# Performance work log

Hardware: AMD Instinct MI355X
Metric: run time of the kernel (lower is better)

## Reference

```python
import jax, jax.numpy as jnp
import numpy as np

N = 20000      # nodes
E = 320000     # edges (before self-loops)
D = 128        # esm_embeds
H = 4          # n_heads (layer 1)
G = 256        # graphs in batch
SLOPE = 0.2    # GATConv default negative_slope


def setup_inputs() -> dict:
    key = jax.random.key(0)
    ks = jax.random.split(key, 16)
    x = jax.random.normal(ks[0], (N, D), jnp.float32)
    src = jax.random.randint(ks[1], (E,), 0, N)
    off = jax.random.randint(ks[2], (E,), 1, N)
    dst = (src + off) % N  # guaranteed no self-loops (PyG removes then re-adds them)
    edge_index = jnp.stack([src, dst]).astype(jnp.int64)
    batch = jnp.sort(jax.random.randint(ks[3], (N,), 0, G)).astype(jnp.int64)
    s = 0.05
    W1 = jax.random.normal(ks[4], (D, H * D), jnp.float32) * s
    a_src1 = jax.random.normal(ks[5], (1, H, D), jnp.float32) * s
    a_dst1 = jax.random.normal(ks[6], (1, H, D), jnp.float32) * s
    b1 = jnp.zeros((H * D,), jnp.float32)
    W2 = jax.random.normal(ks[7], (H * D, D), jnp.float32) * s
    a_src2 = jax.random.normal(ks[8], (1, 1, D), jnp.float32) * s
    a_dst2 = jax.random.normal(ks[9], (1, 1, D), jnp.float32) * s
    b2 = jnp.zeros((D,), jnp.float32)
    fc1_w = jax.random.normal(ks[10], (D, 16), jnp.float32) * s
    fc1_b = jnp.zeros((16,), jnp.float32)
    fc2_w = jax.random.normal(ks[11], (16, 1), jnp.float32) * s
    fc2_b = jnp.zeros((1,), jnp.float32)
    return {"x": x, "edge_index": edge_index, "batch": batch,
            "W1": W1, "a_src1": a_src1, "a_dst1": a_dst1, "b1": b1,
            "W2": W2, "a_src2": a_src2, "a_dst2": a_dst2, "b2": b2,
            "fc1_w": fc1_w, "fc1_b": fc1_b, "fc2_w": fc2_w, "fc2_b": fc2_b}


def _gat_conv(h, src, dst, a_src, a_dst, n):
    """h: [n, heads, C]; returns aggregated [n, heads, C] (PyG GATConv message passing)."""
    al_s = jnp.sum(h * a_src, axis=-1)  # [n, heads]
    al_d = jnp.sum(h * a_dst, axis=-1)  # [n, heads]
    e = jax.nn.leaky_relu(al_s[src] + al_d[dst], SLOPE)  # [Etot, heads]
    m = jax.lax.stop_gradient(jax.ops.segment_max(e, dst, num_segments=n))
    ex = jnp.exp(e - m[dst])
    denom = jax.ops.segment_sum(ex, dst, num_segments=n)
    alpha = ex / denom[dst]                               # per-destination softmax
    msg = h[src] * alpha[..., None]                       # [Etot, heads, C]
    return jax.ops.segment_sum(msg, dst, num_segments=n)


def reference(x, edge_index, batch, W1, a_src1, a_dst1, b1,
              W2, a_src2, a_dst2, b2, fc1_w, fc1_b, fc2_w, fc2_b):
    n = x.shape[0]
    loop = jnp.arange(n, dtype=edge_index.dtype)
    src = jnp.concatenate([edge_index[0], loop])  # GATConv add_self_loops=True
    dst = jnp.concatenate([edge_index[1], loop])
    # layer 1: heads=H, concat -> [n, H*D], then ELU (dropout is identity in eval)
    h1 = (x @ W1).reshape(n, H, D)
    o1 = _gat_conv(h1, src, dst, a_src1, a_dst1, n).reshape(n, H * D) + b1
    x1 = jax.nn.elu(o1)
    # layer 2: heads=1, concat -> [n, D], then ReLU
    h2 = (x1 @ W2).reshape(n, 1, D)
    o2 = _gat_conv(h2, src, dst, a_src2, a_dst2, n).reshape(n, D) + b2
    x2 = jax.nn.relu(o2)
    # global max pool over graphs; x2 >= 0 so clamping handles any empty segment
    pooled = jnp.maximum(jax.ops.segment_max(x2, batch, num_segments=G), 0.0)
    hfc = jax.nn.relu(pooled @ fc1_w + fc1_b)
    return hfc @ fc2_w + fc2_b  # [G, 1]
```

## Files before the change

### kernel.cpp

```cpp
#include <hip/hip_runtime.h>
#include <hip/hip_fp16.h>

#define N_NODES 20000
#define E_EDGES 320000
#define D_DIM   128
#define H1HEADS 4
#define G_GRAPHS 256
#define SLOPE   0.2f

typedef _Float16 h8 __attribute__((ext_vector_type(8)));
typedef float float4v __attribute__((ext_vector_type(4)));

__global__ void cnt_k(const int* __restrict__ dst, int* __restrict__ cnt) {
    int e = blockIdx.x * blockDim.x + threadIdx.x;
    if (e < E_EDGES) atomicAdd(&cnt[dst[e]], 1);
}

__global__ __launch_bounds__(256) void scan_k(const int* __restrict__ cnt,
                                              int* __restrict__ rowptr) {
    __shared__ int s[256];
    const int t = threadIdx.x;
    const int CH = (N_NODES + 255) / 256;
    int base = t * CH;
    int sum = 0;
    for (int i = 0; i < CH; ++i) {
        int idx = base + i;
        if (idx < N_NODES) sum += cnt[idx];
    }
    s[t] = sum;
    __syncthreads();
    for (int off = 1; off < 256; off <<= 1) {
        int v = (t >= off) ? s[t - off] : 0;
        __syncthreads();
        s[t] += v;
        __syncthreads();
    }
    int run = (t > 0) ? s[t - 1] : 0;
    for (int i = 0; i < CH; ++i) {
        int idx = base + i;
        if (idx < N_NODES) { rowptr[idx] = run; run += cnt[idx]; }
    }
    if (t == 255) rowptr[N_NODES] = run;
}

__global__ void scat_k(const int* __restrict__ src, const int* __restrict__ dst,
                       const int* __restrict__ rowptr, int* __restrict__ cur,
                       int* __restrict__ csrsrc) {
    int e = blockIdx.x * blockDim.x + threadIdx.x;
    if (e >= E_EDGES) return;
    int d = dst[e];
    int p = rowptr[d] + atomicAdd(&cur[d], 1);
    csrsrc[p] = src[e];
}

__device__ __forceinline__ int bitonic64(int key, int lane) {
#pragma unroll
    for (int k = 2; k <= 64; k <<= 1) {
#pragma unroll
        for (int j = k >> 1; j > 0; j >>= 1) {
            int other = __shfl_xor(key, j);
            bool up = ((lane & k) == 0);
            bool lower = ((lane & j) == 0);
            int mn = min(key, other), mx = max(key, other);
            key = (up == lower) ? mn : mx;
        }
    }
    return key;
}

__global__ __launch_bounds__(256) void sortb_k(const int* __restrict__ rowptr,
                                               int* __restrict__ csrsrc) {
    const int node = (blockIdx.x * blockDim.x + threadIdx.x) >> 6;
    if (node >= N_NODES) return;
    const int lane = threadIdx.x & 63;
    const int r0 = rowptr[node];
    const int deg = rowptr[node + 1] - r0;
    if (deg <= 1 || deg > 64) return;
    int key = 0x7FFFFFFF;
    if (lane < deg) key = csrsrc[r0 + lane];
    key = bitonic64(key, lane);
    if (lane < deg) csrsrc[r0 + lane] = key;
}

__global__ void splitall_k(const float* __restrict__ x, __half* __restrict__ xhi,
                           __half* __restrict__ xlo,
                           const float* __restrict__ W1, __half* __restrict__ w1t,
                           const float* __restrict__ W2, __half* __restrict__ w2t) {
    int i = blockIdx.x * blockDim.x + threadIdx.x;
    if (i < N_NODES * 128) {
        float v = x[i];
        __half h = __float2half(v);
        xhi[i] = h;
        xlo[i] = __float2half(v - __half2float(h));
    }
    if (i < 128 * 512) {
        {
            int k = i >> 9, n = i & 511;
            w1t[n * 128 + k] = __float2half(W1[i]);
        }
        {
            int k = i >> 7, n = i & 127;
            w2t[n * 512 + k] = __float2half(W2[i]);
        }
    }
}

__device__ __forceinline__ void store_val(__half* p, float v) { *p = __float2half(v); }
__device__ __forceinline__ void store_val(float* p, float v) { *p = v; }

template <typename OT>
__global__ __launch_bounds__(256) void fgemm_k(const __half* __restrict__ Ahi,
                                               const __half* __restrict__ Alo,
                                               const __half* __restrict__ BT,
                                               const int M, const int N, const int K,
                                               OT* __restrict__ C) {
    constexpr int SA = 72;
    __shared__ __half Ah[64 * SA], Al[64 * SA];
    const int t = threadIdx.x;
    const int wave = t >> 6, lane = t & 63;
    const int q = lane >> 4, rr = lane & 15;
    const int row0 = blockIdx.x * 64;
    const int col0 = blockIdx.y * 128;
    const int wm = wave & 1, wn = wave >> 1;

    float4v acc[2][4];
#pragma unroll
    for (int i = 0; i < 2; ++i)
#pragma unroll
        for (int j = 0; j < 4; ++j) acc[i][j] = (float4v){0.f, 0.f, 0.f, 0.f};

    for (int kc = 0; kc < K; kc += 64) {
        __syncthreads();
#pragma unroll
        for (int i = 0; i < 2; ++i) {
            int u = t + i * 256;
            int m = u >> 3, mac = u & 7;
            int r = row0 + m;
            uint4 vh = make_uint4(0, 0, 0, 0), vl = make_uint4(0, 0, 0, 0);
            if (r < M) {
                vh = *(const uint4*)(Ahi + (size_t)r * K + kc + mac * 8);
                vl = *(const uint4*)(Alo + (size_t)r * K + kc + mac * 8);
            }
            *(uint4*)(Ah + m * SA + mac * 8) = vh;
            *(uint4*)(Al + m * SA + mac * 8) = vl;
        }
        __syncthreads();
#pragma unroll
        for (int ks = 0; ks < 2; ++ks) {
            const int ko = ks * 32 + q * 8;
            h8 ah[2], alo[2], bh[4];
#pragma unroll
            for (int mt = 0; mt < 2; ++mt) {
                int m = (wm * 2 + mt) * 16 + rr;
                ah[mt]  = *(const h8*)(Ah + m * SA + ko);
                alo[mt] = *(const h8*)(Al + m * SA + ko);
            }
#pragma unroll
            for (int nt = 0; nt < 4; ++nt) {
                int n = (wn * 4 + nt) * 16 + rr;
                bh[nt] = *(const h8*)(BT + (size_t)(col0 + n) * K + kc + ko);
            }
#pragma unroll
            for (int mt = 0; mt < 2; ++mt)
#pragma unroll
                for (int nt = 0; nt < 4; ++nt) {
                    acc[mt][nt] = __builtin_amdgcn_mfma_f32_16x16x32_f16(
                        ah[mt], bh[nt], acc[mt][nt], 0, 0, 0);
                    acc[mt][nt] = __builtin_amdgcn_mfma_f32_16x16x32_f16(
                        alo[mt], bh[nt], acc[mt][nt], 0, 0, 0);
                }
        }
    }
#pragma unroll
    for (int mt = 0; mt < 2; ++mt) {
#pragma unroll
        for (int reg = 0; reg < 4; ++reg) {
            int r = row0 + (wm * 2 + mt) * 16 + q * 4 + reg;
            if (r < M) {
#pragma unroll
                for (int nt = 0; nt < 4; ++nt) {
                    int c = col0 + (wn * 4 + nt) * 16 + rr;
                    store_val(&C[(size_t)r * N + c], acc[mt][nt][reg]);
                }
            }
        }
    }
}

__global__ __launch_bounds__(256) void al16_k(const __half* __restrict__ h,
                                              const float* __restrict__ a_src,
                                              const float* __restrict__ a_dst,
                                              float* __restrict__ als,
                                              float* __restrict__ ald,
                                              const int NH, const int H) {
    int wid = (blockIdx.x * blockDim.x + threadIdx.x) >> 6;
    int lane = threadIdx.x & 63;
    if (wid >= NH) return;
    int hh = wid % H;
    const __half2* row = (const __half2*)(h + (size_t)wid * 128);
    float2 v = __half22float2(row[lane]);
    float2 as2 = ((const float2*)(a_src + hh * 128))[lane];
    float2 ad2 = ((const float2*)(a_dst + hh * 128))[lane];
    float s = v.x * as2.x + v.y * as2.y;
    float d = v.x * ad2.x + v.y * ad2.y;
#pragma unroll
    for (int off = 32; off > 0; off >>= 1) {
        s += __shfl_down(s, off);
        d += __shfl_down(d, off);
    }
    if (lane == 0) { als[wid] = s; ald[wid] = d; }
}

__device__ __forceinline__ float lrelu(float v) { return (v > 0.f) ? v : SLOPE * v; }

__global__ __launch_bounds__(256) void agg1_k(const __half* __restrict__ h,
                                              const float4* __restrict__ als4,
                                              const float4* __restrict__ ald4,
                                              const int* __restrict__ rowptr,
                                              const int* __restrict__ csrsrc,
                                              const float* __restrict__ bias,
                                              __half* __restrict__ x1hi,
                                              __half* __restrict__ x1lo) {
    __shared__ int   ss[4][64];
    __shared__ float ws[4][64][4];
    const int node = (blockIdx.x * blockDim.x + threadIdx.x) >> 6;
    if (node >= N_NODES) return;
    const int lane = threadIdx.x & 63;
    const int wv = threadIdx.x >> 6;
    const int head = lane >> 4;
    const int r0 = rowptr[node];
    const int deg = rowptr[node + 1] - r0;
    const int tot = deg + 1;
    const float4 aldn = ald4[node];

    float acc[8] = {};
    float4 d4;

    if (tot <= 64) {
        int s = node;
        if (lane < deg) s = csrsrc[r0 + lane];
        float4 l4 = make_float4(-1e30f, -1e30f, -1e30f, -1e30f);
        if (lane < tot) {
            float4 a = als4[s];
            l4.x = lrelu(a.x + aldn.x); l4.y = lrelu(a.y + aldn.y);
            l4.z = lrelu(a.z + aldn.z); l4.w = lrelu(a.w + aldn.w);
        }
        float4 m4 = l4;
#pragma unroll
        for (int off = 32; off > 0; off >>= 1) {
            m4.x = fmaxf(m4.x, __shfl_xor(m4.x, off));
            m4.y = fmaxf(m4.y, __shfl_xor(m4.y, off));
            m4.z = fmaxf(m4.z, __shfl_xor(m4.z, off));
            m4.w = fmaxf(m4.w, __shfl_xor(m4.w, off));
        }
        float4 w4 = make_float4(0.f, 0.f, 0.f, 0.f);
        if (lane < tot) {
            w4.x = expf(l4.x - m4.x); w4.y = expf(l4.y - m4.y);
            w4.z = expf(l4.z - m4.z); w4.w = expf(l4.w - m4.w);
        }
        d4 = w4;
#pragma unroll
        for (int off = 32; off > 0; off >>= 1) {
            d4.x += __shfl_xor(d4.x, off);
            d4.y += __shfl_xor(d4.y, off);
            d4.z += __shfl_xor(d4.z, off);
            d4.w += __shfl_xor(d4.w, off);
        }
        ss[wv][lane] = s;
        *(float4*)&ws[wv][lane][0] = w4;
        for (int j = 0; j < tot; ++j) {
            int sj = ss[wv][j];
            float wj = ws[wv][j][head];
            const uint4 pk = *((const uint4*)(h + (size_t)sj * 512) + lane);
            const __half2* p2 = (const __half2*)&pk;
            float2 f0 = __half22float2(p2[0]);
            float2 f1 = __half22float2(p2[1]);
            float2 f2 = __half22float2(p2[2]);
            float2 f3 = __half22float2(p2[3]);
            acc[0] += wj * f0.x; acc[1] += wj * f0.y;
            acc[2] += wj * f1.x; acc[3] += wj * f1.y;
            acc[4] += wj * f2.x; acc[5] += wj * f2.y;
            acc[6] += wj * f3.x; acc[7] += wj * f3.y;
        }
    } else {
        float4 m4 = make_float4(-1e30f, -1e30f, -1e30f, -1e30f);
        for (int base = 0; base < tot; base += 64) {
            int j = base + lane;
            float4 l4 = make_float4(-1e30f, -1e30f, -1e30f, -1e30f);
            if (j < tot) {
                int s = (j < deg) ? csrsrc[r0 + j] : node;
                float4 a = als4[s];
                l4.x = lrelu(a.x + aldn.x); l4.y = lrelu(a.y + aldn.y);
                l4.z = lrelu(a.z + aldn.z); l4.w = lrelu(a.w + aldn.w);
            }
#pragma unroll
            for (int off = 32; off > 0; off >>= 1) {
                l4.x = fmaxf(l4.x, __shfl_xor(l4.x, off));
                l4.y = fmaxf(l4.y, __shfl_xor(l4.y, off));
                l4.z = fmaxf(l4.z, __shfl_xor(l4.z, off));
                l4.w = fmaxf(l4.w, __shfl_xor(l4.w, off));
            }
            m4.x = fmaxf(m4.x, l4.x); m4.y = fmaxf(m4.y, l4.y);
            m4.z = fmaxf(m4.z, l4.z); m4.w = fmaxf(m4.w, l4.w);
        }
        d4 = make_float4(0.f, 0.f, 0.f, 0.f);
        for (int base = 0; base < tot; base += 64) {
            int j = base + lane;
            int s = node;
            float4 w4 = make_float4(0.f, 0.f, 0.f, 0.f);
            if (j < tot) {
                if (j < deg) s = csrsrc[r0 + j];
                float4 a = als4[s];
                w4.x = expf(lrelu(a.x + aldn.x) - m4.x);
                w4.y = expf(lrelu(a.y + aldn.y) - m4.y);
                w4.z = expf(lrelu(a.z + aldn.z) - m4.z);
                w4.w = expf(lrelu(a.w + aldn.w) - m4.w);
            }
            float4 p4 = w4;
#pragma unroll
            for (int off = 32; off > 0; off >>= 1) {
                p4.x += __shfl_xor(p4.x, off);
                p4.y += __shfl_xor(p4.y, off);
                p4.z += __shfl_xor(p4.z, off);
                p4.w += __shfl_xor(p4.w, off);
            }
            d4.x += p4.x; d4.y += p4.y; d4.z += p4.z; d4.w += p4.w;
            int lim = min(64, tot - base);
            for (int j2 = 0; j2 < lim; ++j2) {
                int sj = __shfl(s, j2);
                float w0 = __shfl(w4.x, j2), w1 = __shfl(w4.y, j2);
                float w2 = __shfl(w4.z, j2), w3 = __shfl(w4.w, j2);
                float wj = (head < 2) ? (head == 0 ? w0 : w1) : (head == 2 ? w2 : w3);
                const uint4 pk = *((const uint4*)(h + (size_t)sj * 512) + lane);
                const __half2* p2 = (const __half2*)&pk;
                float2 f0 = __half22float2(p2[0]);
                float2 f1 = __half22float2(p2[1]);
                float2 f2 = __half22float2(p2[2]);
                float2 f3 = __half22float2(p2[3]);
                acc[0] += wj * f0.x; acc[1] += wj * f0.y;
                acc[2] += wj * f1.x; acc[3] += wj * f1.y;
                acc[4] += wj * f2.x; acc[5] += wj * f2.y;
                acc[6] += wj * f3.x; acc[7] += wj * f3.y;
            }
        }
    }

    const float dsel = (head < 2) ? (head == 0 ? d4.x : d4.y) : (head == 2 ? d4.z : d4.w);
    const float inv = 1.f / dsel;
    const float4 b0 = ((const float4*)bias)[lane * 2];
    const float4 b1 = ((const float4*)bias)[lane * 2 + 1];
    float v[8];
    v[0] = acc[0] * inv + b0.x; v[1] = acc[1] * inv + b0.y;
    v[2] = acc[2] * inv + b0.z; v[3] = acc[3] * inv + b0.w;
    v[4] = acc[4] * inv + b1.x; v[5] = acc[5] * inv + b1.y;
    v[6] = acc[6] * inv + b1.z; v[7] = acc[7] * inv + b1.w;
    uint4 ph, pl;
    __half* hps = (__half*)&ph;
    __half* lps = (__half*)&pl;
#pragma unroll
    for (int k = 0; k < 8; ++k) {
        float e = (v[k] > 0.f) ? v[k] : expm1f(v[k]);
        __half hb = __float2half(e);
        hps[k] = hb;
        lps[k] = __float2half(e - __half2float(hb));
    }
    *(uint4*)(x1hi + (size_t)node * 512 + lane * 8) = ph;
    *(uint4*)(x1lo + (size_t)node * 512 + lane * 8) = pl;
}

__global__ __launch_bounds__(256) void agg2_k(const __half* __restrict__ h,
                                              const float* __restrict__ als,
                                              const float* __restrict__ ald,
                                              const int* __restrict__ rowptr,
                                              const int* __restrict__ csrsrc,
                                              const float* __restrict__ bias,
                                              const int* __restrict__ batch,
                                              int* __restrict__ pooled) {
    __shared__ int   ss[4][64];
    __shared__ float ws[4][64];
    const int node = (blockIdx.x * blockDim.x + threadIdx.x) >> 6;
    if (node >= N_NODES) return;
    const int lane = threadIdx.x & 63;
    const int wv = threadIdx.x >> 6;
    const int r0 = rowptr[node];
    const int deg = rowptr[node + 1] - r0;
    const int tot = deg + 1;
    const float aldn = ald[node];

    float acc0 = 0.f, acc1 = 0.f;
    float denom;

    if (tot <= 64) {
        int s = node;
        if (lane < deg) s = csrsrc[r0 + lane];
        float l = -1e30f, w = 0.f;
        if (lane < tot) l = lrelu(als[s] + aldn);
        float m = l;
#pragma unroll
        for (int off = 32; off > 0; off >>= 1) m = fmaxf(m, __shfl_xor(m, off));
        if (lane < tot) w = expf(l - m);
        denom = w;
#pragma unroll
        for (int off = 32; off > 0; off >>= 1) denom += __shfl_xor(denom, off);
        ss[wv][lane] = s;
        ws[wv][lane] = w;
        for (int j = 0; j < tot; ++j) {
            int sj = ss[wv][j];
            float wj = ws[wv][j];
            float2 f = __half22float2(((const __half2*)(h + (size_t)sj * 128))[lane]);
            acc0 += wj * f.x;
            acc1 += wj * f.y;
        }
    } else {
        float m = -1e30f;
        for (int base = 0; base < tot; base += 64) {
            int j = base + lane;
            float l = -1e30f;
            if (j < tot) {
                int s = (j < deg) ? csrsrc[r0 + j] : node;
                l = lrelu(als[s] + aldn);
            }
#pragma unroll
            for (int off = 32; off > 0; off >>= 1) l = fmaxf(l, __shfl_xor(l, off));
            m = fmaxf(m, l);
        }
        denom = 0.f;
        for (int base = 0; base < tot; base += 64) {
            int j = base + lane;
            int s = node;
            float w = 0.f;
            if (j < tot) {
                if (j < deg) s = csrsrc[r0 + j];
                w = expf(lrelu(als[s] + aldn) - m);
            }
            float ws2 = w;
#pragma unroll
            for (int off = 32; off > 0; off >>= 1) ws2 += __shfl_xor(ws2, off);
            denom += ws2;
            int lim = min(64, tot - base);
            for (int j2 = 0; j2 < lim; ++j2) {
                int sj = __shfl(s, j2);
                float wj = __shfl(w, j2);
                float2 f = __half22float2(((const __half2*)(h + (size_t)sj * 128))[lane]);
                acc0 += wj * f.x;
                acc1 += wj * f.y;
            }
        }
    }

    const float inv = 1.f / denom;
    float v0 = fmaxf(acc0 * inv + bias[lane * 2], 0.f);
    float v1 = fmaxf(acc1 * inv + bias[lane * 2 + 1], 0.f);
    int* pb = pooled + batch[node] * 128;
    atomicMax(&pb[lane * 2], __float_as_int(v0));
    atomicMax(&pb[lane * 2 + 1], __float_as_int(v1));
}

__global__ __launch_bounds__(64) void fc_k(const float* __restrict__ pooled,
                                           const float* __restrict__ w1,
                                           const float* __restrict__ b1,
                                           const float* __restrict__ w2,
                                           const float* __restrict__ b2,
                                           float* __restrict__ out) {
    int g = blockIdx.x;
    __shared__ float p[128];
    int t = threadIdx.x;
    p[t] = pooled[g * 128 + t];
    p[t + 64] = pooled[g * 128 + 64 + t];
    __syncthreads();
    float acc = 0.f;
    if (t < 16) {
        float s = b1[t];
        for (int c = 0; c < 128; ++c) s += p[c] * w1[c * 16 + t];
        s = fmaxf(s, 0.f);
        acc = s * w2[t];
    }
#pragma unroll
    for (int off = 8; off > 0; off >>= 1) acc += __shfl_down(acc, off);
    if (t == 0) out[g] = acc + b2[0];
}

extern "C" void kernel_launch(void* const* d_in, const int* in_sizes, int n_in,
                              void* d_out, int out_size, void* d_ws, size_t ws_size,
                              hipStream_t stream) {
    const float* x      = (const float*)d_in[0];
    const int*   ei     = (const int*)d_in[1];
    const int*   batch  = (const int*)d_in[2];
    const float* W1     = (const float*)d_in[3];
    const float* a_src1 = (const float*)d_in[4];
    const float* a_dst1 = (const float*)d_in[5];
    const float* b1     = (const float*)d_in[6];
    const float* W2     = (const float*)d_in[7];
    const float* a_src2 = (const float*)d_in[8];
    const float* a_dst2 = (const float*)d_in[9];
    const float* b2     = (const float*)d_in[10];
    const float* fc1w   = (const float*)d_in[11];
    const float* fc1b   = (const float*)d_in[12];
    const float* fc2w   = (const float*)d_in[13];
    const float* fc2b   = (const float*)d_in[14];
    float* out = (float*)d_out;

    const int* src = ei;
    const int* dst = ei + E_EDGES;

    int*   cnt    = (int*)d_ws;
    int*   cur    = cnt + 20000;
    int*   pooled = cur + 20000;
    int*   rowptr = pooled + 32768;
    int*   csrsrc = rowptr + 20004;
    __half* h1h   = (__half*)(csrsrc + 320000);
    __half* h2h   = h1h + 10240000;
    float* als1   = (float*)(h2h + 2560000);
    float* ald1   = als1 + 80000;
    float* als2   = ald1 + 80000;
    float* ald2   = als2 + 20000;
    __half* xhi   = (__half*)(ald2 + 20000);
    __half* xlo   = xhi + 2560000;
    __half* w1t   = xlo + 2560000;
    __half* w2t   = w1t + 65536;
    __half* x1hi  = w2t + 65536;
    __half* x1lo  = x1hi + 10240000;

    (void)hipMemsetAsync(d_ws, 0, 72768 * 4, stream);

    cnt_k<<<(E_EDGES + 255) / 256, 256, 0, stream>>>(dst, cnt);
    scan_k<<<1, 256, 0, stream>>>(cnt, rowptr);
    scat_k<<<(E_EDGES + 255) / 256, 256, 0, stream>>>(src, dst, rowptr, cur, csrsrc);
    sortb_k<<<N_NODES / 4, 256, 0, stream>>>(rowptr, csrsrc);

    splitall_k<<<(N_NODES * 128 + 255) / 256, 256, 0, stream>>>(
        x, xhi, xlo, W1, w1t, W2, w2t);

    fgemm_k<__half><<<dim3(313, 4), 256, 0, stream>>>(xhi, xlo, w1t,
                                                      N_NODES, 512, 128, h1h);

    al16_k<<<(N_NODES * H1HEADS) / 4, 256, 0, stream>>>(h1h, a_src1, a_dst1, als1, ald1,
                                                        N_NODES * H1HEADS, H1HEADS);

    agg1_k<<<N_NODES / 4, 256, 0, stream>>>(h1h, (const float4*)als1, (const float4*)ald1,
                                            rowptr, csrsrc, b1, x1hi, x1lo);

    fgemm_k<__half><<<dim3(313, 1), 256, 0, stream>>>(x1hi, x1lo, w2t,
                                                      N_NODES, 128, 512, h2h);

    al16_k<<<N_NODES / 4, 256, 0, stream>>>(h2h, a_src2, a_dst2, als2, ald2, N_NODES, 1);

    agg2_k<<<N_NODES / 4, 256, 0, stream>>>(h2h, als2, ald2, rowptr, csrsrc, b2,
                                            batch, pooled);

    fc_k<<<G_GRAPHS, 64, 0, stream>>>((const float*)pooled, fc1w, fc1b, fc2w, fc2b, out);
}
```

Baseline: 325.2 us.

## Fuse fp16 split into GEMM, fuse attention logits into GEMM epilogue, parallelize scan

The GEMM now reads fp32 activations and does the hi/lo fp16 split while staging tiles in shared memory. That removes the separate split kernel and the hi/lo buffers, and agg1 now writes fp32 output directly. The attention dot products (als/ald) are computed in the GEMM epilogue from the fp32 accumulators, which replaces the al16 kernels. The single-block scan becomes a three-kernel multi-block scan, and the aggregation loops prefetch four neighbour rows ahead. In exchange, the GEMM reads twice the activation bytes per tile, its epilogue gains extra shuffles and a barrier, and the logits are now taken from unrounded fp32 values rather than the stored fp16 ones.

```diff
diff --git a/kernel.cpp b/kernel.cpp
--- a/kernel.cpp
+++ b/kernel.cpp
@@ -16,31 +16,44 @@
     if (e < E_EDGES) atomicAdd(&cnt[dst[e]], 1);
 }
 
-__global__ __launch_bounds__(256) void scan_k(const int* __restrict__ cnt,
-                                              int* __restrict__ rowptr) {
+#define SCAN_B 79
+__global__ __launch_bounds__(256) void scan1_k(const int* __restrict__ cnt,
+                                               int* __restrict__ part) {
     __shared__ int s[256];
-    const int t = threadIdx.x;
-    const int CH = (N_NODES + 255) / 256;
-    int base = t * CH;
-    int sum = 0;
-    for (int i = 0; i < CH; ++i) {
-        int idx = base + i;
-        if (idx < N_NODES) sum += cnt[idx];
-    }
-    s[t] = sum;
+    int t = threadIdx.x;
+    int i = blockIdx.x * 256 + t;
+    int v = (i < N_NODES) ? cnt[i] : 0;
+    s[t] = v;
+    __syncthreads();
+    for (int off = 128; off > 0; off >>= 1) {
+        if (t < off) s[t] += s[t + off];
+        __syncthreads();
+    }
+    if (t == 0) part[blockIdx.x] = s[0];
+}
+__global__ void scan2_k(int* __restrict__ part) {
+    if (threadIdx.x == 0) {
+        int run = 0;
+        for (int b = 0; b < SCAN_B; ++b) { int v = part[b]; part[b] = run; run += v; }
+    }
+}
+__global__ __launch_bounds__(256) void scan3_k(const int* __restrict__ cnt,
+                                               const int* __restrict__ part,
+                                               int* __restrict__ rowptr) {
+    __shared__ int s[256];
+    int t = threadIdx.x;
+    int i = blockIdx.x * 256 + t;
+    int v = (i < N_NODES) ? cnt[i] : 0;
+    s[t] = v;
     __syncthreads();
     for (int off = 1; off < 256; off <<= 1) {
-        int v = (t >= off) ? s[t - off] : 0;
+        int u = (t >= off) ? s[t - off] : 0;
         __syncthreads();
-        s[t] += v;
+        s[t] += u;
         __syncthreads();
     }
-    int run = (t > 0) ? s[t - 1] : 0;
-    for (int i = 0; i < CH; ++i) {
-        int idx = base + i;
-        if (idx < N_NODES) { rowptr[idx] = run; run += cnt[idx]; }
-    }
-    if (t == 255) rowptr[N_NODES] = run;
+    if (i < N_NODES) rowptr[i] = part[blockIdx.x] + s[t] - v;
+    if (blockIdx.x == 0 && t == 0) rowptr[N_NODES] = E_EDGES;
 }
 
 __global__ void scat_k(const int* __restrict__ src, const int* __restrict__ dst,
@@ -82,26 +95,17 @@
     if (lane < deg) csrsrc[r0 + lane] = key;
 }
 
-__global__ void splitall_k(const float* __restrict__ x, __half* __restrict__ xhi,
-                           __half* __restrict__ xlo,
-                           const float* __restrict__ W1, __half* __restrict__ w1t,
-                           const float* __restrict__ W2, __half* __restrict__ w2t) {
+__global__ void prepw_k(const float* __restrict__ W1, __half* __restrict__ w1t,
+                        const float* __restrict__ W2, __half* __restrict__ w2t) {
     int i = blockIdx.x * blockDim.x + threadIdx.x;
-    if (i < N_NODES * 128) {
-        float v = x[i];
-        __half h = __float2half(v);
-        xhi[i] = h;
-        xlo[i] = __float2half(v - __half2float(h));
-    }
-    if (i < 128 * 512) {
-        {
-            int k = i >> 9, n = i & 511;
-            w1t[n * 128 + k] = __float2half(W1[i]);
-        }
-        {
-            int k = i >> 7, n = i & 127;
-            w2t[n * 512 + k] = __float2half(W2[i]);
-        }
+    if (i >= 128 * 512) return;
+    {
+        int k = i >> 9, n = i & 511;
+        w1t[n * 128 + k] = __float2half(W1[i]);
+    }
+    {
+        int k = i >> 7, n = i & 127;
+        w2t[n * 512 + k] = __float2half(W2[i]);
     }
 }
 
@@ -109,19 +113,24 @@
 __device__ __forceinline__ void store_val(float* p, float v) { *p = v; }
 
 template <typename OT>
-__global__ __launch_bounds__(256) void fgemm_k(const __half* __restrict__ Ahi,
-                                               const __half* __restrict__ Alo,
+__global__ __launch_bounds__(256) void fgemm_k(const float* __restrict__ A,
                                                const __half* __restrict__ BT,
                                                const int M, const int N, const int K,
-                                               OT* __restrict__ C) {
+                                               OT* __restrict__ C,
+                                               float* __restrict__ als,
+                                               float* __restrict__ ald,
+                                               const float* __restrict__ asrc,
+                                               const float* __restrict__ adst) {
     constexpr int SA = 72;
     __shared__ __half Ah[64 * SA], Al[64 * SA];
+    __shared__ float sdot[64][2][2];
     const int t = threadIdx.x;
     const int wave = t >> 6, lane = t & 63;
     const int q = lane >> 4, rr = lane & 15;
     const int row0 = blockIdx.x * 64;
     const int col0 = blockIdx.y * 128;
     const int wm = wave & 1, wn = wave >> 1;
+    const int H = gridDim.y;
 
     float4v acc[2][4];
 #pragma unroll
@@ -132,17 +141,22 @@
     for (int kc = 0; kc < K; kc += 64) {
         __syncthreads();
 #pragma unroll
-        for (int i = 0; i < 2; ++i) {
+        for (int i = 0; i < 4; ++i) {
             int u = t + i * 256;
-            int m = u >> 3, mac = u & 7;
+            int m = u >> 4, mac = u & 15;
             int r = row0 + m;
-            uint4 vh = make_uint4(0, 0, 0, 0), vl = make_uint4(0, 0, 0, 0);
-            if (r < M) {
-                vh = *(const uint4*)(Ahi + (size_t)r * K + kc + mac * 8);
-                vl = *(const uint4*)(Alo + (size_t)r * K + kc + mac * 8);
-            }
-            *(uint4*)(Ah + m * SA + mac * 8) = vh;
-            *(uint4*)(Al + m * SA + mac * 8) = vl;
+            float4 fv = make_float4(0.f, 0.f, 0.f, 0.f);
+            if (r < M) fv = *(const float4*)(A + (size_t)r * K + kc + mac * 4);
+            union { __half h[4]; uint2 u2; } ph, pl;
+            float f[4] = {fv.x, fv.y, fv.z, fv.w};
+#pragma unroll
+            for (int k = 0; k < 4; ++k) {
+                __half hb = __float2half(f[k]);
+                ph.h[k] = hb;
+                pl.h[k] = __float2half(f[k] - __half2float(hb));
+            }
+            *(uint2*)(Ah + m * SA + mac * 4) = ph.u2;
+            *(uint2*)(Al + m * SA + mac * 4) = pl.u2;
         }
         __syncthreads();
 #pragma unroll
@@ -185,30 +199,42 @@
             }
         }
     }
-}
-
-__global__ __launch_bounds__(256) void al16_k(const __half* __restrict__ h,
-                                              const float* __restrict__ a_src,
-                                              const float* __restrict__ a_dst,
-                                              float* __restrict__ als,
-                                              float* __restrict__ ald,
-                                              const int NH, const int H) {
-    int wid = (blockIdx.x * blockDim.x + threadIdx.x) >> 6;
-    int lane = threadIdx.x & 63;
-    if (wid >= NH) return;
-    int hh = wid % H;
-    const __half2* row = (const __half2*)(h + (size_t)wid * 128);
-    float2 v = __half22float2(row[lane]);
-    float2 as2 = ((const float2*)(a_src + hh * 128))[lane];
-    float2 ad2 = ((const float2*)(a_dst + hh * 128))[lane];
-    float s = v.x * as2.x + v.y * as2.y;
-    float d = v.x * ad2.x + v.y * ad2.y;
-#pragma unroll
-    for (int off = 32; off > 0; off >>= 1) {
-        s += __shfl_down(s, off);
-        d += __shfl_down(d, off);
-    }
-    if (lane == 0) { als[wid] = s; ald[wid] = d; }
+    ((float*)sdot)[t] = 0.f;
+    __syncthreads();
+    const float* as = asrc + blockIdx.y * 128;
+    const float* ad = adst + blockIdx.y * 128;
+#pragma unroll
+    for (int mt = 0; mt < 2; ++mt) {
+#pragma unroll
+        for (int reg = 0; reg < 4; ++reg) {
+            float ps = 0.f, pd = 0.f;
+#pragma unroll
+            for (int nt = 0; nt < 4; ++nt) {
+                int cc = (wn * 4 + nt) * 16 + rr;
+                float v = acc[mt][nt][reg];
+                ps += v * as[cc];
+                pd += v * ad[cc];
+            }
+#pragma unroll
+            for (int off = 1; off < 16; off <<= 1) {
+                ps += __shfl_xor(ps, off);
+                pd += __shfl_xor(pd, off);
+            }
+            if (rr == 0) {
+                int row = (wm * 2 + mt) * 16 + q * 4 + reg;
+                sdot[row][wn][0] = ps;
+                sdot[row][wn][1] = pd;
+            }
+        }
+    }
+    __syncthreads();
+    if (t < 64) {
+        int r = row0 + t;
+        if (r < M) {
+            als[r * H + blockIdx.y] = sdot[t][0][0] + sdot[t][1][0];
+            ald[r * H + blockIdx.y] = sdot[t][0][1] + sdot[t][1][1];
+        }
+    }
 }
 
 __device__ __forceinline__ float lrelu(float v) { return (v > 0.f) ? v : SLOPE * v; }
@@ -219,8 +245,7 @@
                                               const int* __restrict__ rowptr,
                                               const int* __restrict__ csrsrc,
                                               const float* __restrict__ bias,
-                                              __half* __restrict__ x1hi,
-                                              __half* __restrict__ x1lo) {
+                                              float* __restrict__ x1) {
     __shared__ int   ss[4][64];
     __shared__ float ws[4][64][4];
     const int node = (blockIdx.x * blockDim.x + threadIdx.x) >> 6;
@@ -268,19 +293,19 @@
         }
         ss[wv][lane] = s;
         *(float4*)&ws[wv][lane][0] = w4;
+        const uint4* hp = (const uint4*)h;
+        uint4 buf[4];
+#pragma unroll
+        for (int i = 0; i < 4; ++i)
+            if (i < tot) buf[i] = hp[(size_t)ss[wv][i] * 64 + lane];
         for (int j = 0; j < tot; ++j) {
-            int sj = ss[wv][j];
+            uint4 pk = buf[j & 3];
+            int jn = j + 4;
+            if (jn < tot) buf[j & 3] = hp[(size_t)ss[wv][jn] * 64 + lane];
             float wj = ws[wv][j][head];
-            const uint4 pk = *((const uint4*)(h + (size_t)sj * 512) + lane);
-            const __half2* p2 = (const __half2*)&pk;
-            float2 f0 = __half22float2(p2[0]);
-            float2 f1 = __half22float2(p2[1]);
-            float2 f2 = __half22float2(p2[2]);
-            float2 f3 = __half22float2(p2[3]);
-            acc[0] += wj * f0.x; acc[1] += wj * f0.y;
-            acc[2] += wj * f1.x; acc[3] += wj * f1.y;
-            acc[4] += wj * f2.x; acc[5] += wj * f2.y;
-            acc[6] += wj * f3.x; acc[7] += wj * f3.y;
+            const __half* p = (const __half*)&pk;
+#pragma unroll
+            for (int k = 0; k < 8; ++k) acc[k] += wj * __half2float(p[k]);
         }
     } else {
         float4 m4 = make_float4(-1e30f, -1e30f, -1e30f, -1e30f);
@@ -332,15 +357,9 @@
                 float w2 = __shfl(w4.z, j2), w3 = __shfl(w4.w, j2);
                 float wj = (head < 2) ? (head == 0 ? w0 : w1) : (head == 2 ? w2 : w3);
                 const uint4 pk = *((const uint4*)(h + (size_t)sj * 512) + lane);
-                const __half2* p2 = (const __half2*)&pk;
-                float2 f0 = __half22float2(p2[0]);
-                float2 f1 = __half22float2(p2[1]);
-                float2 f2 = __half22float2(p2[2]);
-                float2 f3 = __half22float2(p2[3]);
-                acc[0] += wj * f0.x; acc[1] += wj * f0.y;
-                acc[2] += wj * f1.x; acc[3] += wj * f1.y;
-                acc[4] += wj * f2.x; acc[5] += wj * f2.y;
-                acc[6] += wj * f3.x; acc[7] += wj * f3.y;
+                const __half* p = (const __half*)&pk;
+#pragma unroll
+                for (int k = 0; k < 8; ++k) acc[k] += wj * __half2float(p[k]);
             }
         }
     }
@@ -354,18 +373,11 @@
     v[2] = acc[2] * inv + b0.z; v[3] = acc[3] * inv + b0.w;
     v[4] = acc[4] * inv + b1.x; v[5] = acc[5] * inv + b1.y;
     v[6] = acc[6] * inv + b1.z; v[7] = acc[7] * inv + b1.w;
-    uint4 ph, pl;
-    __half* hps = (__half*)&ph;
-    __half* lps = (__half*)&pl;
-#pragma unroll
-    for (int k = 0; k < 8; ++k) {
-        float e = (v[k] > 0.f) ? v[k] : expm1f(v[k]);
-        __half hb = __float2half(e);
-        hps[k] = hb;
-        lps[k] = __float2half(e - __half2float(hb));
-    }
-    *(uint4*)(x1hi + (size_t)node * 512 + lane * 8) = ph;
-    *(uint4*)(x1lo + (size_t)node * 512 + lane * 8) = pl;
+#pragma unroll
+    for (int k = 0; k < 8; ++k) v[k] = (v[k] > 0.f) ? v[k] : expm1f(v[k]);
+    float4* orow = (float4*)(x1 + (size_t)node * 512);
+    orow[lane * 2]     = make_float4(v[0], v[1], v[2], v[3]);
+    orow[lane * 2 + 1] = make_float4(v[4], v[5], v[6], v[7]);
 }
 
 __global__ __launch_bounds__(256) void agg2_k(const __half* __restrict__ h,
@@ -404,12 +416,19 @@
         for (int off = 32; off > 0; off >>= 1) denom += __shfl_xor(denom, off);
         ss[wv][lane] = s;
         ws[wv][lane] = w;
+        const unsigned* hp = (const unsigned*)h;
+        unsigned buf[4];
+#pragma unroll
+        for (int i = 0; i < 4; ++i)
+            if (i < tot) buf[i] = hp[(size_t)ss[wv][i] * 64 + lane];
         for (int j = 0; j < tot; ++j) {
-            int sj = ss[wv][j];
+            unsigned pk = buf[j & 3];
+            int jn = j + 4;
+            if (jn < tot) buf[j & 3] = hp[(size_t)ss[wv][jn] * 64 + lane];
             float wj = ws[wv][j];
-            float2 f = __half22float2(((const __half2*)(h + (size_t)sj * 128))[lane]);
-            acc0 += wj * f.x;
-            acc1 += wj * f.y;
+            __half2 hh = *(__half2*)&pk;
+            acc0 += wj * __half2float(hh.x);
+            acc1 += wj * __half2float(hh.y);
         }
     } else {
         float m = -1e30f;
@@ -507,43 +526,37 @@
     int*   cur    = cnt + 20000;
     int*   pooled = cur + 20000;
     int*   rowptr = pooled + 32768;
-    int*   csrsrc = rowptr + 20004;
+    int*   part   = rowptr + 20004;
+    int*   csrsrc = part + 128;
     __half* h1h   = (__half*)(csrsrc + 320000);
     __half* h2h   = h1h + 10240000;
     float* als1   = (float*)(h2h + 2560000);
     float* ald1   = als1 + 80000;
     float* als2   = ald1 + 80000;
     float* ald2   = als2 + 20000;
-    __half* xhi   = (__half*)(ald2 + 20000);
-    __half* xlo   = xhi + 2560000;
-    __half* w1t   = xlo + 2560000;
+    __half* w1t   = (__half*)(ald2 + 20000);
     __half* w2t   = w1t + 65536;
-    __half* x1hi  = w2t + 65536;
-    __half* x1lo  = x1hi + 10240000;
+    float* x1     = (float*)(w2t + 65536);
 
     (void)hipMemsetAsync(d_ws, 0, 72768 * 4, stream);
 
     cnt_k<<<(E_EDGES + 255) / 256, 256, 0, stream>>>(dst, cnt);
-    scan_k<<<1, 256, 0, stream>>>(cnt, rowptr);
+    scan1_k<<<SCAN_B, 256, 0, stream>>>(cnt, part);
+    scan2_k<<<1, 64, 0, stream>>>(part);
+    scan3_k<<<SCAN_B, 256, 0, stream>>>(cnt, part, rowptr);
     scat_k<<<(E_EDGES + 255) / 256, 256, 0, stream>>>(src, dst, rowptr, cur, csrsrc);
     sortb_k<<<N_NODES / 4, 256, 0, stream>>>(rowptr, csrsrc);
 
-    splitall_k<<<(N_NODES * 128 + 255) / 256, 256, 0, stream>>>(
-        x, xhi, xlo, W1, w1t, W2, w2t);
-
-    fgemm_k<__half><<<dim3(313, 4), 256, 0, stream>>>(xhi, xlo, w1t,
-                                                      N_NODES, 512, 128, h1h);
-
-    al16_k<<<(N_NODES * H1HEADS) / 4, 256, 0, stream>>>(h1h, a_src1, a_dst1, als1, ald1,
-                                                        N_NODES * H1HEADS, H1HEADS);
+    prepw_k<<<(128 * 512 + 255) / 256, 256, 0, stream>>>(W1, w1t, W2, w2t);
+
+    fgemm_k<__half><<<dim3(313, 4), 256, 0, stream>>>(x, w1t, N_NODES, 512, 128, h1h,
+                                                      als1, ald1, a_src1, a_dst1);
 
     agg1_k<<<N_NODES / 4, 256, 0, stream>>>(h1h, (const float4*)als1, (const float4*)ald1,
-                                            rowptr, csrsrc, b1, x1hi, x1lo);
-
-    fgemm_k<__half><<<dim3(313, 1), 256, 0, stream>>>(x1hi, x1lo, w2t,
-                                                      N_NODES, 128, 512, h2h);
-
-    al16_k<<<N_NODES / 4, 256, 0, stream>>>(h2h, a_src2, a_dst2, als2, ald2, N_NODES, 1);
+                                            rowptr, csrsrc, b1, x1);
+
+    fgemm_k<__half><<<dim3(313, 1), 256, 0, stream>>>(x1, w2t, N_NODES, 128, 512, h2h,
+                                                      als2, ald2, a_src2, a_dst2);
 
     agg2_k<<<N_NODES / 4, 256, 0, stream>>>(h2h, als2, ald2, rowptr, csrsrc, b2,
                                             batch, pooled);
```

After: 390.7 us. 1.2x slower.
